# Optimization experiments

Hardware: AMD Instinct MI355X
Metric: run time of the kernel (lower is better)

Reference implementation:

```python
import jax, jax.numpy as jnp
import numpy as np

HEAD_NUM = 8


def setup_inputs() -> dict:
    key = jax.random.key(0)
    k1, k2, k3, k4 = jax.random.split(key, 4)
    B, S, F = 16, 512, 512
    H = HEAD_NUM
    x = jax.random.normal(k1, (B, S, F), dtype=jnp.float32)
    # keras initializer 'normal' ~ small random normal weights
    wq = jax.random.normal(k2, (F, S * H), dtype=jnp.float32) * 0.05
    wk = jax.random.normal(k3, (F, S * H), dtype=jnp.float32) * 0.05
    wv = jax.random.normal(k4, (F, S * H), dtype=jnp.float32) * 0.05
    return {"x": x, "wq": wq, "wk": wk, "wv": wv}


def _split_heads(t, H):
    # tf.stack(tf.split(t, H, axis=2)): [B,S,H*S] -> [H,B,S,S]
    B, S, D = t.shape
    return t.reshape(B, S, H, D // H).transpose(2, 0, 1, 3)


def reference(x, wq, wk, wv):
    H = HEAD_NUM
    B, S, F = x.shape
    q = _split_heads(jnp.einsum('bsf,fd->bsd', x, wq), H)  # [H,B,S,S]
    k = _split_heads(jnp.einsum('bsf,fd->bsd', x, wk), H)
    v = _split_heads(jnp.einsum('bsf,fd->bsd', x, wv), H)
    # NOTE: no 1/sqrt(d) scaling in the original module
    scores = jax.nn.softmax(jnp.einsum('hbid,hbjd->hbij', q, k), axis=-1)
    eff = jnp.einsum('hbij,hbjd->hbid', scores, v)  # [H,B,S,S]
    # tf.concat(tf.split(eff, H), axis=-1) + squeeze: [H,B,S,S] -> [B,S,H*S]
    return eff.transpose(1, 2, 0, 3).reshape(B, S, H * S)
```

## Files before the change

### kernel.cpp

```cpp
#include <hip/hip_runtime.h>


typedef unsigned short u16;
typedef __bf16 bf16x8 __attribute__((ext_vector_type(8)));
typedef unsigned short u16x4 __attribute__((ext_vector_type(4)));
typedef unsigned short u16x8s __attribute__((ext_vector_type(8)));
typedef float f32x4 __attribute__((ext_vector_type(4)));

typedef __attribute__((address_space(1))) void gvoid_t;
typedef __attribute__((address_space(3))) void svoid_t;

__device__ __forceinline__ u16 f2bf(float f) {
  unsigned u = __float_as_uint(f);
  u = (u + 0x7fffu + ((u >> 16) & 1u)) >> 16;
  return (u16)u;
}
__device__ __forceinline__ float bf2f(u16 h) {
  return __uint_as_float(((unsigned)h) << 16);
}

__device__ __forceinline__ f32x4 mfma16(bf16x8 a, bf16x8 b, f32x4 c) {
  return __builtin_amdgcn_mfma_f32_16x16x32_bf16(a, b, c, 0, 0, 0);
}

__global__ __launch_bounds__(256) void split_hl_kernel(
    const float* __restrict__ in, u16* __restrict__ hi, u16* __restrict__ lo,
    int n4) {
  int i = blockIdx.x * 256 + threadIdx.x;
  if (i >= n4) return;
  float4 v = ((const float4*)in)[i];
  float vv[4] = {v.x, v.y, v.z, v.w};
  u16x4 h, l;
#pragma unroll
  for (int j = 0; j < 4; ++j) {
    u16 hh = f2bf(vv[j]);
    h[j] = hh;
    l[j] = f2bf(vv[j] - bf2f(hh));
  }
  ((u16x4*)hi)[i] = h;
  ((u16x4*)lo)[i] = l;
}

__global__ __launch_bounds__(256) void transpose_split_w(
    const float* __restrict__ in, u16* __restrict__ hi, u16* __restrict__ lo) {
  __shared__ float t[32][33];
  int d0 = blockIdx.x * 32, f0 = blockIdx.y * 32;
  int tx = threadIdx.x, ty = threadIdx.y;
#pragma unroll
  for (int r = 0; r < 4; ++r)
    t[ty + r * 8][tx] = in[(size_t)(f0 + ty + r * 8) * 4096 + d0 + tx];
  __syncthreads();
#pragma unroll
  for (int r = 0; r < 4; ++r) {
    float v = t[tx][ty + r * 8];
    int d = d0 + ty + r * 8, f = f0 + tx;
    u16 h = f2bf(v);
    size_t idx = (size_t)d * 512 + f;
    hi[idx] = h;
    lo[idx] = f2bf(v - bf2f(h));
  }
}

__device__ __forceinline__ bf16x8 ldsfrag(const u16* tile, int row, int quad) {
  int c = quad ^ ((row >> 1) & 3);
  return *(const bf16x8*)(tile + row * 32 + c * 8);
}

__device__ __forceinline__ void stage_tile(u16* ldsTile, const u16* g0, int ld,
                                           int wave, int lane) {
#pragma unroll
  for (int r = 0; r < 2; ++r) {
    int p = r * 256 + wave * 64 + lane;
    int m = p >> 2;
    int cq = (p & 3) ^ ((m >> 1) & 3);
    const u16* g = g0 + (size_t)m * ld + cq * 8;
    u16* l = ldsTile + (size_t)(r * 256 + wave * 64) * 8;
    __builtin_amdgcn_global_load_lds((gvoid_t*)g, (svoid_t*)l, 16, 0, 0);
  }
}

template <int SPLIT, int OMODE>
__global__ __launch_bounds__(256, 2) void gemm_bt(
    const u16* __restrict__ Ah, const u16* __restrict__ Al,
    const u16* __restrict__ Bh, const u16* __restrict__ Bl,
    void* __restrict__ C0, void* __restrict__ C1, int lda, int ldb, int ldc,
    int K, size_t aH, size_t aB, size_t bH, size_t bB, size_t cH, size_t cB) {
  __shared__ __align__(16) u16 lds[(SPLIT ? 4 : 2) * 4096];
  u16* lAh = lds;
  u16* lAl = SPLIT ? (lds + 4096) : lds;
  u16* lBh = lds + (SPLIT ? 8192 : 4096);
  u16* lBl = SPLIT ? (lds + 12288) : lds;

  const int zh = blockIdx.z >> 4, zb = blockIdx.z & 15;
  Ah += zh * aH + zb * aB;
  Al += zh * aH + zb * aB;
  Bh += zh * bH + zb * bB;
  Bl += zh * bH + zb * bB;
  const size_t cOff = zh * cH + zb * cB;

  const int m0 = blockIdx.y * 128, n0 = blockIdx.x * 128;
  const int tid = threadIdx.x;
  const int wave = tid >> 6, lane = tid & 63;
  const int quad = lane >> 4, l16 = lane & 15;
  const int wm = (wave >> 1) * 64, wn = (wave & 1) * 64;

  f32x4 acc[4][4] = {};

  for (int k0 = 0; k0 < K; k0 += 32) {
    stage_tile(lAh, Ah + (size_t)m0 * lda + k0, lda, wave, lane);
    if (SPLIT) stage_tile(lAl, Al + (size_t)m0 * lda + k0, lda, wave, lane);
    stage_tile(lBh, Bh + (size_t)n0 * ldb + k0, ldb, wave, lane);
    if (SPLIT) stage_tile(lBl, Bl + (size_t)n0 * ldb + k0, ldb, wave, lane);
    __syncthreads();

    bf16x8 a_h[4], a_l[4], b_h[4], b_l[4];
#pragma unroll
    for (int i = 0; i < 4; ++i) {
      a_h[i] = ldsfrag(lAh, wm + i * 16 + l16, quad);
      b_h[i] = ldsfrag(lBh, wn + i * 16 + l16, quad);
      if (SPLIT) {
        a_l[i] = ldsfrag(lAl, wm + i * 16 + l16, quad);
        b_l[i] = ldsfrag(lBl, wn + i * 16 + l16, quad);
      }
    }
#pragma unroll
    for (int i = 0; i < 4; ++i)
#pragma unroll
      for (int j = 0; j < 4; ++j) {
        acc[i][j] = mfma16(a_h[i], b_h[j], acc[i][j]);
        if (SPLIT) {
          acc[i][j] = mfma16(a_h[i], b_l[j], acc[i][j]);
          acc[i][j] = mfma16(a_l[i], b_h[j], acc[i][j]);
        }
      }
    __syncthreads();
  }

#pragma unroll
  for (int i = 0; i < 4; ++i) {
#pragma unroll
    for (int j = 0; j < 4; ++j) {
      int col = n0 + wn + j * 16 + l16;
#pragma unroll
      for (int r = 0; r < 4; ++r) {
        int row = m0 + wm + i * 16 + quad * 4 + r;
        size_t idx = cOff + (size_t)row * ldc + col;
        float v = acc[i][j][r];
        if (OMODE == 0) {
          ((float*)C0)[idx] = v;
        } else if (OMODE == 1) {
          ((u16*)C0)[idx] = f2bf(v);
        } else {
          u16 h = f2bf(v);
          ((u16*)C0)[idx] = h;
          ((u16*)C1)[idx] = f2bf(v - bf2f(h));
        }
      }
    }
  }
}

__device__ __forceinline__ void stage256(u16* tile, const u16* g0, int ld,
                                         int tid) {
  const int wave = tid >> 6;
#pragma unroll
  for (int r = 0; r < 2; ++r) {
    int p = r * 512 + tid;
    int m = p >> 2;
    int cq = (p & 3) ^ ((m >> 1) & 3);
    const u16* g = g0 + (size_t)m * ld + cq * 8;
    u16* l = tile + (size_t)(r * 512 + wave * 64) * 8;
    __builtin_amdgcn_global_load_lds((gvoid_t*)g, (svoid_t*)l, 16, 0, 0);
  }
}

template <int SPLIT>
__device__ __forceinline__ void stage_all256(u16* buf, const u16* Ah,
                                             const u16* Al, const u16* Bh,
                                             const u16* Bl, int lda, int ldb,
                                             int m0, int n0, int k0, int tid) {
  stage256(buf, Ah + (size_t)m0 * lda + k0, lda, tid);
  if (SPLIT) stage256(buf + 8192, Al + (size_t)m0 * lda + k0, lda, tid);
  stage256(buf + (SPLIT ? 16384 : 8192), Bh + (size_t)n0 * ldb + k0, ldb, tid);
  if (SPLIT) stage256(buf + 24576, Bl + (size_t)n0 * ldb + k0, ldb, tid);
}

template <int SPLIT, int OMODE>
__global__ __launch_bounds__(512, 2) void gemm256(
    const u16* __restrict__ Ah, const u16* __restrict__ Al,
    const u16* __restrict__ Bh, const u16* __restrict__ Bl,
    void* __restrict__ C0, void* __restrict__ C1, int lda, int ldb, int ldc,
    int K, size_t aH, size_t aB, size_t bH, size_t bB, size_t cH, size_t cB) {
  constexpr int BUF = (SPLIT ? 4 : 2) * 8192;
  __shared__ __align__(16) u16 lds[2 * BUF];

  const int gx = gridDim.x, gy = gridDim.y;
  const int nb = gx * gy * (int)gridDim.z;
  int orig = blockIdx.x + gx * (blockIdx.y + gy * blockIdx.z);
  int swz = orig;
  if ((nb & 7) == 0) swz = (orig & 7) * (nb >> 3) + (orig >> 3);
  const int bx = swz % gx;
  const int byz = swz / gx;
  const int by = byz % gy;
  const int bz = byz / gy;

  const int zh = bz >> 4, zb = bz & 15;
  Ah += zh * aH + zb * aB;
  Al += zh * aH + zb * aB;
  Bh += zh * bH + zb * bB;
  Bl += zh * bH + zb * bB;
  const size_t cOff = zh * cH + zb * cB;

  const int m0 = by * 256, n0 = bx * 256;
  const int tid = threadIdx.x;
  const int wave = tid >> 6, lane = tid & 63;
  const int quad = lane >> 4, l16 = lane & 15;
  const int wm = (wave >> 2) * 128, wn = (wave & 3) * 64;

  f32x4 acc[8][4] = {};

  stage_all256<SPLIT>(lds, Ah, Al, Bh, Bl, lda, ldb, m0, n0, 0, tid);
  __syncthreads();

  int cur = 0;
  for (int k0 = 0; k0 < K; k0 += 32) {
    if (k0 + 32 < K)
      stage_all256<SPLIT>(lds + (cur ^ 1) * BUF, Ah, Al, Bh, Bl, lda, ldb, m0,
                          n0, k0 + 32, tid);

    u16* lA_h = lds + cur * BUF;
    u16* lA_l = lA_h + 8192;
    u16* lB_h = lA_h + (SPLIT ? 16384 : 8192);
    u16* lB_l = lA_h + 24576;

    bf16x8 bhf[4], blf[4];
#pragma unroll
    for (int j = 0; j < 4; ++j) {
      bhf[j] = ldsfrag(lB_h, wn + j * 16 + l16, quad);
      if (SPLIT) blf[j] = ldsfrag(lB_l, wn + j * 16 + l16, quad);
    }
#pragma unroll
    for (int i = 0; i < 8; ++i) {
      bf16x8 ah = ldsfrag(lA_h, wm + i * 16 + l16, quad);
      bf16x8 al;
      if (SPLIT) al = ldsfrag(lA_l, wm + i * 16 + l16, quad);
#pragma unroll
      for (int j = 0; j < 4; ++j) {
        acc[i][j] = mfma16(ah, bhf[j], acc[i][j]);
        if (SPLIT) {
          acc[i][j] = mfma16(ah, blf[j], acc[i][j]);
          acc[i][j] = mfma16(al, bhf[j], acc[i][j]);
        }
      }
    }
    __syncthreads();
    cur ^= 1;
  }

#pragma unroll
  for (int i = 0; i < 8; ++i) {
#pragma unroll
    for (int j = 0; j < 4; ++j) {
      int col = n0 + wn + j * 16 + l16;
#pragma unroll
      for (int r = 0; r < 4; ++r) {
        int row = m0 + wm + i * 16 + quad * 4 + r;
        size_t idx = cOff + (size_t)row * ldc + col;
        float v = acc[i][j][r];
        if (OMODE == 0) {
          ((float*)C0)[idx] = v;
        } else if (OMODE == 1) {
          ((u16*)C0)[idx] = f2bf(v);
        } else {
          u16 h = f2bf(v);
          ((u16*)C0)[idx] = h;
          ((u16*)C1)[idx] = f2bf(v - bf2f(h));
        }
      }
    }
  }
}

__global__ __launch_bounds__(256) void softmax_rows(
    const float* __restrict__ in, u16* __restrict__ out) {
  int row = blockIdx.x * 4 + (threadIdx.x >> 6);
  int lane = threadIdx.x & 63;
  const float* p = in + (size_t)row * 512 + lane * 8;
  float4 v0 = *(const float4*)p;
  float4 v1 = *(const float4*)(p + 4);
  float v[8] = {v0.x, v0.y, v0.z, v0.w, v1.x, v1.y, v1.z, v1.w};
  float m = v[0];
#pragma unroll
  for (int i = 1; i < 8; ++i) m = fmaxf(m, v[i]);
#pragma unroll
  for (int o = 32; o > 0; o >>= 1) m = fmaxf(m, __shfl_xor(m, o));
  float s = 0.f;
#pragma unroll
  for (int i = 0; i < 8; ++i) {
    v[i] = __expf(v[i] - m);
    s += v[i];
  }
#pragma unroll
  for (int o = 32; o > 0; o >>= 1) s += __shfl_xor(s, o);
  float inv = 1.0f / s;
  u16x8s rr;
#pragma unroll
  for (int i = 0; i < 8; ++i) rr[i] = f2bf(v[i] * inv);
  *(u16x8s*)(out + (size_t)row * 512 + lane * 8) = rr;
}

extern "C" void kernel_launch(void* const* d_in, const int* in_sizes, int n_in,
                              void* d_out, int out_size, void* d_ws,
                              size_t ws_size, hipStream_t stream) {
  const float* x = (const float*)d_in[0];
  const float* wq = (const float*)d_in[1];
  const float* wk = (const float*)d_in[2];
  const float* wv = (const float*)d_in[3];
  float* out = (float*)d_out;
  char* ws = (char*)d_ws;

  const size_t MB = 1024ull * 1024ull;
  u16* XHI = (u16*)(ws + 0 * MB);
  u16* XLO = (u16*)(ws + 8 * MB);
  u16* WQH = (u16*)(ws + 16 * MB);
  u16* WQL = (u16*)(ws + 20 * MB);
  u16* WKH = (u16*)(ws + 24 * MB);
  u16* WKL = (u16*)(ws + 28 * MB);
  u16* WVTH = (u16*)(ws + 32 * MB);
  u16* WVTL = (u16*)(ws + 36 * MB);
  u16* MPH = (u16*)(ws + 40 * MB);
  u16* MPL = (u16*)(ws + 44 * MB);
  u16* THI = (u16*)(ws + 48 * MB);
  u16* TLO = (u16*)(ws + 112 * MB);
  u16* VT = (u16*)(ws + 176 * MB);
  float* LOG = (float*)(ws + 240 * MB);
  u16* P = THI;

  split_hl_kernel<<<4096, 256, 0, stream>>>(x, XHI, XLO, 1048576);
  split_hl_kernel<<<2048, 256, 0, stream>>>(wq, WQH, WQL, 524288);
  split_hl_kernel<<<2048, 256, 0, stream>>>(wk, WKH, WKL, 524288);
  transpose_split_w<<<dim3(128, 16), dim3(32, 8), 0, stream>>>(wv, WVTH, WVTL);

  gemm_bt<1, 2><<<dim3(4, 4, 8), 256, 0, stream>>>(
      WKH, WKL, WQH, WQL, MPH, MPL, 4096, 4096, 512, 512,
       0,  512,  0,  512,  0,  262144);

  gemm256<1, 2><<<dim3(2, 32, 8), 512, 0, stream>>>(
      XHI, XLO, MPH, MPL, THI, TLO, 512, 512, 512, 512,
      0, 0, 0, 262144, 0, 4194304);

  gemm256<0, 1><<<dim3(32, 16, 1), 512, 0, stream>>>(
      WVTH, WVTH, XHI, XHI, VT, nullptr, 512, 512, 8192, 512,
      0, 0, 0, 0, 0, 0);

  gemm256<1, 0><<<dim3(2, 2, 128), 512, 0, stream>>>(
      THI, TLO, XHI, XLO, LOG, nullptr, 512, 512, 512, 512,
       4194304,  262144,  0,  262144,
       4194304,  262144);

  softmax_rows<<<16384, 256, 0, stream>>>(LOG, P);

  gemm256<0, 0><<<dim3(2, 2, 128), 512, 0, stream>>>(
      P, P, VT, VT, out, nullptr, 512, 8192, 4096, 512,
       4194304,  262144,  4194304,  512,
       512,  2097152);
}
```

Measured before the change: 512.9 us.

## Interleave next-tile staging with MFMA phases using barriers and setprio

Splits each K-step of the 256x256 GEMM main loop into phases. Each phase loads a slice of A fragments, issues one quarter or half of the next tile's global-to-LDS staging, then runs its MFMAs at raised wave priority. The goal is to spread memory traffic across the compute so loads overlap with MFMA execution instead of being issued as one burst. The cost is extra per-phase s_barriers and an explicit vmcnt wait. It also relies on stage256 being async (LDS direct loads), otherwise the ordering may be wrong.

Measured after the change: 530.0 us. 3.3% more time.

```diff
diff --git a/kernel.cpp b/kernel.cpp
--- a/kernel.cpp
+++ b/kernel.cpp
@@ -222,38 +222,72 @@
   stage_all256<SPLIT>(lds, Ah, Al, Bh, Bl, lda, ldb, m0, n0, 0, tid);
   __syncthreads();
 
+  constexpr int IC = SPLIT ? 2 : 4;
+  constexpr int NPH = 8 / IC;
+
   int cur = 0;
   for (int k0 = 0; k0 < K; k0 += 32) {
-    if (k0 + 32 < K)
-      stage_all256<SPLIT>(lds + (cur ^ 1) * BUF, Ah, Al, Bh, Bl, lda, ldb, m0,
-                          n0, k0 + 32, tid);
-
-    u16* lA_h = lds + cur * BUF;
-    u16* lA_l = lA_h + 8192;
-    u16* lB_h = lA_h + (SPLIT ? 16384 : 8192);
-    u16* lB_l = lA_h + 24576;
+    u16* buf = lds + cur * BUF;
+    u16* nbuf = lds + (cur ^ 1) * BUF;
+    const bool pf = (k0 + 32 < K);
+    const int k1 = k0 + 32;
+
+    u16* lA_h = buf;
+    u16* lA_l = buf + 8192;
+    u16* lB_h = buf + (SPLIT ? 16384 : 8192);
+    u16* lB_l = buf + 24576;
 
     bf16x8 bhf[4], blf[4];
 #pragma unroll
-    for (int j = 0; j < 4; ++j) {
-      bhf[j] = ldsfrag(lB_h, wn + j * 16 + l16, quad);
-      if (SPLIT) blf[j] = ldsfrag(lB_l, wn + j * 16 + l16, quad);
+    for (int ph = 0; ph < NPH; ++ph) {
+      if (ph == 0) {
+#pragma unroll
+        for (int j = 0; j < 4; ++j) {
+          bhf[j] = ldsfrag(lB_h, wn + j * 16 + l16, quad);
+          if (SPLIT) blf[j] = ldsfrag(lB_l, wn + j * 16 + l16, quad);
+        }
+      }
+      bf16x8 ah[IC], al[IC];
+#pragma unroll
+      for (int u = 0; u < IC; ++u) {
+        int i = ph * IC + u;
+        ah[u] = ldsfrag(lA_h, wm + i * 16 + l16, quad);
+        if (SPLIT) al[u] = ldsfrag(lA_l, wm + i * 16 + l16, quad);
+      }
+      if (pf) {
+        if (SPLIT) {
+          if (ph == 0) stage256(nbuf, Ah + (size_t)m0 * lda + k1, lda, tid);
+          if (ph == 1)
+            stage256(nbuf + 8192, Al + (size_t)m0 * lda + k1, lda, tid);
+          if (ph == 2)
+            stage256(nbuf + 16384, Bh + (size_t)n0 * ldb + k1, ldb, tid);
+          if (ph == 3)
+            stage256(nbuf + 24576, Bl + (size_t)n0 * ldb + k1, ldb, tid);
+        } else {
+          if (ph == 0) stage256(nbuf, Ah + (size_t)m0 * lda + k1, lda, tid);
+          if (ph == 1)
+            stage256(nbuf + 8192, Bh + (size_t)n0 * ldb + k1, ldb, tid);
+        }
+      }
+      __builtin_amdgcn_s_barrier();
+      __builtin_amdgcn_s_setprio(1);
+#pragma unroll
+      for (int u = 0; u < IC; ++u) {
+        int i = ph * IC + u;
+#pragma unroll
+        for (int j = 0; j < 4; ++j) {
+          acc[i][j] = mfma16(ah[u], bhf[j], acc[i][j]);
+          if (SPLIT) {
+            acc[i][j] = mfma16(ah[u], blf[j], acc[i][j]);
+            acc[i][j] = mfma16(al[u], bhf[j], acc[i][j]);
+          }
+        }
+      }
+      __builtin_amdgcn_s_setprio(0);
+      if (ph < NPH - 1) __builtin_amdgcn_s_barrier();
     }
-#pragma unroll
-    for (int i = 0; i < 8; ++i) {
-      bf16x8 ah = ldsfrag(lA_h, wm + i * 16 + l16, quad);
-      bf16x8 al;
-      if (SPLIT) al = ldsfrag(lA_l, wm + i * 16 + l16, quad);
-#pragma unroll
-      for (int j = 0; j < 4; ++j) {
-        acc[i][j] = mfma16(ah, bhf[j], acc[i][j]);
-        if (SPLIT) {
-          acc[i][j] = mfma16(ah, blf[j], acc[i][j]);
-          acc[i][j] = mfma16(al, bhf[j], acc[i][j]);
-        }
-      }
-    }
-    __syncthreads();
+    if (pf) asm volatile("s_waitcnt vmcnt(0)" ::: "memory");
+    __builtin_amdgcn_s_barrier();
     cur ^= 1;
   }
 
```

## Split GEMM k-loop into half-steps with staggered A/B prefetch and partial vmcnt waits

Applied to the files above, without the earlier changes.

Restructures the double-buffered GEMM main loop so A and B tiles live in separate ping-pong regions. The A tile for the next step is prefetched at the start of each iteration, while B is prefetched two steps ahead in mid-iteration after the first half of the MFMAs. Partial s_waitcnt vmcnt waits and raw s_barrier replace full __syncthreads, so global loads stay in flight across barriers. This aims to hide global-to-LDS latency better, at the cost of fragile hand-counted wait counts and an extra barrier per iteration.

Measured after the change: 522.2 us. About the same (+1.8%).

```diff
diff --git a/kernel.cpp b/kernel.cpp
--- a/kernel.cpp
+++ b/kernel.cpp
@@ -174,25 +174,14 @@
   }
 }
 
-template <int SPLIT>
-__device__ __forceinline__ void stage_all256(u16* buf, const u16* Ah,
-                                             const u16* Al, const u16* Bh,
-                                             const u16* Bl, int lda, int ldb,
-                                             int m0, int n0, int k0, int tid) {
-  stage256(buf, Ah + (size_t)m0 * lda + k0, lda, tid);
-  if (SPLIT) stage256(buf + 8192, Al + (size_t)m0 * lda + k0, lda, tid);
-  stage256(buf + (SPLIT ? 16384 : 8192), Bh + (size_t)n0 * ldb + k0, ldb, tid);
-  if (SPLIT) stage256(buf + 24576, Bl + (size_t)n0 * ldb + k0, ldb, tid);
-}
-
 template <int SPLIT, int OMODE>
 __global__ __launch_bounds__(512, 2) void gemm256(
     const u16* __restrict__ Ah, const u16* __restrict__ Al,
     const u16* __restrict__ Bh, const u16* __restrict__ Bl,
     void* __restrict__ C0, void* __restrict__ C1, int lda, int ldb, int ldc,
     int K, size_t aH, size_t aB, size_t bH, size_t bB, size_t cH, size_t cB) {
-  constexpr int BUF = (SPLIT ? 4 : 2) * 8192;
-  __shared__ __align__(16) u16 lds[2 * BUF];
+  constexpr int REG = (SPLIT ? 2 : 1) * 8192;
+  __shared__ __align__(16) u16 lds[4 * REG];
 
   const int gx = gridDim.x, gy = gridDim.y;
   const int nb = gx * gy * (int)gridDim.z;
@@ -217,21 +206,53 @@
   const int quad = lane >> 4, l16 = lane & 15;
   const int wm = (wave >> 2) * 128, wn = (wave & 3) * 64;
 
+  const u16* gA_h = Ah + (size_t)m0 * lda;
+  const u16* gA_l = Al + (size_t)m0 * lda;
+  const u16* gB_h = Bh + (size_t)n0 * ldb;
+  const u16* gB_l = Bl + (size_t)n0 * ldb;
+
+#define STAGE_A(dst, kk)                                  \
+  do {                                                    \
+    stage256((dst), gA_h + (kk), lda, tid);               \
+    if (SPLIT) stage256((dst) + 8192, gA_l + (kk), lda, tid); \
+  } while (0)
+#define STAGE_B(dst, kk)                                  \
+  do {                                                    \
+    stage256((dst), gB_h + (kk), ldb, tid);               \
+    if (SPLIT) stage256((dst) + 8192, gB_l + (kk), ldb, tid); \
+  } while (0)
+#define WAIT_VM_PART()                                             \
+  do {                                                             \
+    if (SPLIT)                                                     \
+      asm volatile("s_waitcnt vmcnt(4)" ::: "memory");             \
+    else                                                           \
+      asm volatile("s_waitcnt vmcnt(2)" ::: "memory");             \
+  } while (0)
+
   f32x4 acc[8][4] = {};
 
-  stage_all256<SPLIT>(lds, Ah, Al, Bh, Bl, lda, ldb, m0, n0, 0, tid);
-  __syncthreads();
-
-  int cur = 0;
-  for (int k0 = 0; k0 < K; k0 += 32) {
-    if (k0 + 32 < K)
-      stage_all256<SPLIT>(lds + (cur ^ 1) * BUF, Ah, Al, Bh, Bl, lda, ldb, m0,
-                          n0, k0 + 32, tid);
-
-    u16* lA_h = lds + cur * BUF;
-    u16* lA_l = lA_h + 8192;
-    u16* lB_h = lA_h + (SPLIT ? 16384 : 8192);
-    u16* lB_l = lA_h + 24576;
+  const int NT = K >> 5;
+
+  STAGE_B(lds + 2 * REG, 0);
+  STAGE_A(lds, 0);
+  if (NT > 1) {
+    STAGE_B(lds + 3 * REG, 32);
+    WAIT_VM_PART();
+  } else {
+    asm volatile("s_waitcnt vmcnt(0)" ::: "memory");
+  }
+  __builtin_amdgcn_s_barrier();
+
+  for (int t = 0; t < NT; ++t) {
+    const int p = t & 1, q = p ^ 1;
+    const int k0 = t << 5;
+    u16* Ap = lds + p * REG;
+    u16* Aq = lds + q * REG;
+    u16* Bp = lds + (2 + p) * REG;
+    u16* lA_h = Ap, *lA_l = Ap + 8192;
+    u16* lB_h = Bp, *lB_l = Bp + 8192;
+
+    if (t + 1 < NT) STAGE_A(Aq, k0 + 32);
 
     bf16x8 bhf[4], blf[4];
 #pragma unroll
@@ -240,7 +261,7 @@
       if (SPLIT) blf[j] = ldsfrag(lB_l, wn + j * 16 + l16, quad);
     }
 #pragma unroll
-    for (int i = 0; i < 8; ++i) {
+    for (int i = 0; i < 4; ++i) {
       bf16x8 ah = ldsfrag(lA_h, wm + i * 16 + l16, quad);
       bf16x8 al;
       if (SPLIT) al = ldsfrag(lA_l, wm + i * 16 + l16, quad);
@@ -253,9 +274,37 @@
         }
       }
     }
-    __syncthreads();
-    cur ^= 1;
-  }
+    asm volatile("s_waitcnt lgkmcnt(0)" ::: "memory");
+    __builtin_amdgcn_sched_barrier(0);
+    __builtin_amdgcn_s_barrier();
+
+    if (t + 2 < NT) STAGE_B(Bp, k0 + 64);
+#pragma unroll
+    for (int i = 4; i < 8; ++i) {
+      bf16x8 ah = ldsfrag(lA_h, wm + i * 16 + l16, quad);
+      bf16x8 al;
+      if (SPLIT) al = ldsfrag(lA_l, wm + i * 16 + l16, quad);
+#pragma unroll
+      for (int j = 0; j < 4; ++j) {
+        acc[i][j] = mfma16(ah, bhf[j], acc[i][j]);
+        if (SPLIT) {
+          acc[i][j] = mfma16(ah, blf[j], acc[i][j]);
+          acc[i][j] = mfma16(al, bhf[j], acc[i][j]);
+        }
+      }
+    }
+    asm volatile("s_waitcnt lgkmcnt(0)" ::: "memory");
+    __builtin_amdgcn_sched_barrier(0);
+    if (t + 2 < NT) {
+      WAIT_VM_PART();
+    } else {
+      asm volatile("s_waitcnt vmcnt(0)" ::: "memory");
+    }
+    __builtin_amdgcn_s_barrier();
+  }
+#undef STAGE_A
+#undef STAGE_B
+#undef WAIT_VM_PART
 
 #pragma unroll
   for (int i = 0; i < 8; ++i) {
```

## Fuse logits GEMM with row softmax into a single kernel

Applied to the files above, without the earlier changes.

Replaces the separate logits GEMM and softmax_rows kernels with one kernel. Each block computes a 128x512 tile of logits, covering full rows, using split-precision bf16 MFMA with double-buffered global-to-LDS loads. It then does the row max, exp and sum reductions through shuffles and LDS, and writes bf16 probabilities directly. This removes the fp32 logits round trip through global memory and one kernel launch. In exchange it uses a large LDS footprint that limits occupancy, and it writes the output with narrow 16-bit scattered stores.

Measured after the change: 499.1 us. 1.03x faster.

```diff
diff --git a/kernel.cpp b/kernel.cpp
--- a/kernel.cpp
+++ b/kernel.cpp
@@ -281,32 +281,152 @@
   }
 }
 
-__global__ __launch_bounds__(256) void softmax_rows(
-    const float* __restrict__ in, u16* __restrict__ out) {
-  int row = blockIdx.x * 4 + (threadIdx.x >> 6);
-  int lane = threadIdx.x & 63;
-  const float* p = in + (size_t)row * 512 + lane * 8;
-  float4 v0 = *(const float4*)p;
-  float4 v1 = *(const float4*)(p + 4);
-  float v[8] = {v0.x, v0.y, v0.z, v0.w, v1.x, v1.y, v1.z, v1.w};
-  float m = v[0];
-#pragma unroll
-  for (int i = 1; i < 8; ++i) m = fmaxf(m, v[i]);
-#pragma unroll
-  for (int o = 32; o > 0; o >>= 1) m = fmaxf(m, __shfl_xor(m, o));
-  float s = 0.f;
-#pragma unroll
-  for (int i = 0; i < 8; ++i) {
-    v[i] = __expf(v[i] - m);
-    s += v[i];
-  }
-#pragma unroll
-  for (int o = 32; o > 0; o >>= 1) s += __shfl_xor(s, o);
-  float inv = 1.0f / s;
-  u16x8s rr;
-#pragma unroll
-  for (int i = 0; i < 8; ++i) rr[i] = f2bf(v[i] * inv);
-  *(u16x8s*)(out + (size_t)row * 512 + lane * 8) = rr;
+__global__ __launch_bounds__(512, 2) void logits_sm(
+    const u16* __restrict__ Th, const u16* __restrict__ Tl,
+    const u16* __restrict__ Xh, const u16* __restrict__ Xl,
+    u16* __restrict__ P, int lda, int ldb,
+    size_t aH, size_t aB, size_t bB, size_t cH, size_t cB) {
+  __shared__ __align__(16) u16 lds[81920];
+
+  const int gx = gridDim.x;
+  const int nb = gx * (int)gridDim.y;
+  int orig = blockIdx.x + gx * blockIdx.y;
+  int swz = orig;
+  if ((nb & 7) == 0) swz = (orig & 7) * (nb >> 3) + (orig >> 3);
+  const int by = swz % gx;
+  const int bz = swz / gx;
+
+  const int zh = bz >> 4, zb = bz & 15;
+  const u16* gA_h = Th + zh * aH + zb * aB;
+  const u16* gA_l = Tl + zh * aH + zb * aB;
+  const u16* gB_h = Xh + zb * bB;
+  const u16* gB_l = Xl + zb * bB;
+  const size_t cOff = zh * cH + zb * cB;
+
+  const int m0 = by * 128;
+  const int tid = threadIdx.x;
+  const int wave = tid >> 6, lane = tid & 63;
+  const int quad = lane >> 4, l16 = lane & 15;
+  const int wn = wave * 64;
+
+  const u16* A_h = gA_h + (size_t)m0 * lda;
+  const u16* A_l = gA_l + (size_t)m0 * lda;
+
+  f32x4 acc[8][4] = {};
+
+  auto STAGE = [&](int b, int kk) {
+    u16* d = lds + b * 40960;
+    {
+      int m = tid >> 2;
+      int cq = (tid & 3) ^ ((m >> 1) & 3);
+      u16* l0 = d + (size_t)(wave * 64) * 8;
+      __builtin_amdgcn_global_load_lds(
+          (gvoid_t*)(A_h + (size_t)m * lda + kk + cq * 8), (svoid_t*)l0, 16, 0,
+          0);
+      __builtin_amdgcn_global_load_lds(
+          (gvoid_t*)(A_l + (size_t)m * lda + kk + cq * 8),
+          (svoid_t*)(l0 + 4096 * 8 / 8 + 0), 16, 0, 0);
+    }
+#pragma unroll
+    for (int r = 0; r < 4; ++r) {
+      int p = r * 512 + tid;
+      int m = p >> 2;
+      int cq = (p & 3) ^ ((m >> 1) & 3);
+      u16* l0 = d + 8192 + (size_t)(r * 512 + wave * 64) * 8;
+      __builtin_amdgcn_global_load_lds(
+          (gvoid_t*)(gB_h + (size_t)m * ldb + kk + cq * 8), (svoid_t*)l0, 16,
+          0, 0);
+      __builtin_amdgcn_global_load_lds(
+          (gvoid_t*)(gB_l + (size_t)m * ldb + kk + cq * 8),
+          (svoid_t*)(l0 + 16384), 16, 0, 0);
+    }
+  };
+
+  STAGE(0, 0);
+  __syncthreads();
+
+  int cur = 0;
+  for (int t = 0; t < 16; ++t) {
+    if (t + 1 < 16) STAGE(cur ^ 1, (t + 1) * 32);
+
+    u16* buf = lds + cur * 40960;
+    u16* lA_h = buf;
+    u16* lA_l = buf + 4096;
+    u16* lB_h = buf + 8192;
+    u16* lB_l = buf + 24576;
+
+    bf16x8 bhf[4], blf[4];
+#pragma unroll
+    for (int j = 0; j < 4; ++j) {
+      bhf[j] = ldsfrag(lB_h, wn + j * 16 + l16, quad);
+      blf[j] = ldsfrag(lB_l, wn + j * 16 + l16, quad);
+    }
+#pragma unroll
+    for (int i = 0; i < 8; ++i) {
+      bf16x8 ah = ldsfrag(lA_h, i * 16 + l16, quad);
+      bf16x8 al = ldsfrag(lA_l, i * 16 + l16, quad);
+#pragma unroll
+      for (int j = 0; j < 4; ++j) {
+        acc[i][j] = mfma16(ah, bhf[j], acc[i][j]);
+        acc[i][j] = mfma16(ah, blf[j], acc[i][j]);
+        acc[i][j] = mfma16(al, bhf[j], acc[i][j]);
+      }
+    }
+    __syncthreads();
+    cur ^= 1;
+  }
+
+  float* smax = (float*)lds;
+  float* ssum = (float*)(lds + 2048);
+
+#pragma unroll
+  for (int i = 0; i < 8; ++i)
+#pragma unroll
+    for (int r = 0; r < 4; ++r) {
+      float m = fmaxf(fmaxf(acc[i][0][r], acc[i][1][r]),
+                      fmaxf(acc[i][2][r], acc[i][3][r]));
+#pragma unroll
+      for (int o = 1; o < 16; o <<= 1) m = fmaxf(m, __shfl_xor(m, o));
+      if (l16 == 0) smax[(i * 16 + quad * 4 + r) * 8 + wave] = m;
+    }
+  __syncthreads();
+
+#pragma unroll
+  for (int i = 0; i < 8; ++i)
+#pragma unroll
+    for (int r = 0; r < 4; ++r) {
+      int row = i * 16 + quad * 4 + r;
+      f32x4 a = *(f32x4*)&smax[row * 8];
+      f32x4 b = *(f32x4*)&smax[row * 8 + 4];
+      float m = fmaxf(fmaxf(fmaxf(a[0], a[1]), fmaxf(a[2], a[3])),
+                      fmaxf(fmaxf(b[0], b[1]), fmaxf(b[2], b[3])));
+      float s = 0.f;
+#pragma unroll
+      for (int j = 0; j < 4; ++j) {
+        float e = __expf(acc[i][j][r] - m);
+        acc[i][j][r] = e;
+        s += e;
+      }
+#pragma unroll
+      for (int o = 1; o < 16; o <<= 1) s += __shfl_xor(s, o);
+      if (l16 == 0) ssum[row * 8 + wave] = s;
+    }
+  __syncthreads();
+
+#pragma unroll
+  for (int i = 0; i < 8; ++i)
+#pragma unroll
+    for (int r = 0; r < 4; ++r) {
+      int row = i * 16 + quad * 4 + r;
+      f32x4 a = *(f32x4*)&ssum[row * 8];
+      f32x4 b = *(f32x4*)&ssum[row * 8 + 4];
+      float s = (a[0] + a[1]) + (a[2] + a[3]) + (b[0] + b[1]) + (b[2] + b[3]);
+      float inv = 1.0f / s;
+      size_t base = cOff + (size_t)(m0 + row) * 512;
+#pragma unroll
+      for (int j = 0; j < 4; ++j)
+        P[base + wn + j * 16 + l16] = f2bf(acc[i][j][r] * inv);
+    }
 }
 
 extern "C" void kernel_launch(void* const* d_in, const int* in_sizes, int n_in,
@@ -333,7 +453,6 @@
   u16* THI = (u16*)(ws + 48 * MB);
   u16* TLO = (u16*)(ws + 112 * MB);
   u16* VT = (u16*)(ws + 176 * MB);
-  float* LOG = (float*)(ws + 240 * MB);
   u16* P = THI;
 
   split_hl_kernel<<<4096, 256, 0, stream>>>(x, XHI, XLO, 1048576);
@@ -353,12 +472,10 @@
       WVTH, WVTH, XHI, XHI, VT, nullptr, 512, 512, 8192, 512,
       0, 0, 0, 0, 0, 0);
 
-  gemm256<1, 0><<<dim3(2, 2, 128), 512, 0, stream>>>(
-      THI, TLO, XHI, XLO, LOG, nullptr, 512, 512, 512, 512,
-       4194304,  262144,  0,  262144,
+  logits_sm<<<dim3(4, 128), 512, 0, stream>>>(
+      THI, TLO, XHI, XLO, P, 512, 512,
+       4194304,  262144,  262144,
        4194304,  262144);
-
-  softmax_rows<<<16384, 256, 0, stream>>>(LOG, P);
 
   gemm256<0, 0><<<dim3(2, 2, 128), 512, 0, stream>>>(
       P, P, VT, VT, out, nullptr, 512, 8192, 4096, 512,
```
